# Kernel tuning notes

Hardware: AMD Instinct MI355X
Metric: run time of the kernel (lower is better)

Reference implementation:

```python
import math
import jax, jax.numpy as jnp
import numpy as np

EPS = 1e-5
NUM_HEADS = 8

def gelu(x):
    return jax.nn.gelu(x, approximate=False)  # keras 'gelu' is exact

def layernorm(x, g, b):
    m = jnp.mean(x, axis=-1, keepdims=True)
    v = jnp.var(x, axis=-1, keepdims=True)
    return (x - m) * jax.lax.rsqrt(v + EPS) * g + b

def setup_inputs() -> dict:
    key = jax.random.key(0)
    ks = jax.random.split(key, 12)
    B, S, N, D = 2, 1, 2048, 256
    E = 256  # dim_emb == dim_out
    s_in = 1.0 / np.sqrt(D).astype(np.float32)
    s_e = 1.0 / np.sqrt(E).astype(np.float32)
    s_h = 1.0 / np.sqrt(4 * E).astype(np.float32)
    return {
        "X": jax.random.normal(ks[0], (B, S, N, D), jnp.float32),
        "Wq": jax.random.normal(ks[1], (D, E), jnp.float32) * s_in,
        "Wk": jax.random.normal(ks[2], (D, E), jnp.float32) * s_in,
        "Wv": jax.random.normal(ks[3], (D, E), jnp.float32) * s_in,
        "Wm": jax.random.normal(ks[4], (E, E), jnp.float32) * s_e,
        "bm": jnp.zeros((E,), jnp.float32),
        "W1": jax.random.normal(ks[5], (E, 4 * E), jnp.float32) * s_e,
        "bf1": jnp.zeros((4 * E,), jnp.float32),
        "W2": jax.random.normal(ks[6], (4 * E, E), jnp.float32) * s_h,
        "bf2": jnp.zeros((E,), jnp.float32),
        "ln0_g": jnp.ones((D,), jnp.float32),
        "ln0_b": jnp.zeros((D,), jnp.float32),
        "ln1_g": jnp.ones((E,), jnp.float32),
        "ln1_b": jnp.zeros((E,), jnp.float32),
    }

def reference(X, Wq, Wk, Wv, Wm, bm, W1, bf1, W2, bf2, ln0_g, ln0_b, ln1_g, ln1_b):
    B, S, N, D = X.shape  # S == 1 (set-transformer singleton axis)
    E = Wq.shape[1]
    H = NUM_HEADS
    dh = E // H
    dim_KV = D  # softmax scale uses dim_KV, not head dim (faithful to source)

    # pre-layer-norm applies only to the Q branch; K/V use raw X
    Xn = layernorm(X, ln0_g, ln0_b)
    Q = Xn @ Wq                      # (B,1,N,E)
    K = X @ Wk
    V = X @ Wv
    X_res = Q                        # fc_res is None -> residual is Q

    def to_heads(T):                 # (B,1,N,E) -> (B,H,N,dh), split along last dim
        return T[:, 0].reshape(B, N, H, dh).transpose(0, 2, 1, 3)

    q, k, v = to_heads(Q), to_heads(K), to_heads(V)
    A = jnp.einsum('bhnd,bhmd->bhnm', q, k) * (1.0 / math.sqrt(dim_KV))  # (B,H,N,N)
    P = jax.nn.softmax(A, axis=-1)
    mh = jnp.einsum('bhnm,bhmd->bhnd', P, v)            # (B,H,N,dh)
    mh = mh.transpose(0, 2, 1, 3).reshape(B, 1, N, E)   # concat heads on last dim

    Hm = gelu(mh @ Wm + bm)          # fc_mix_heads has gelu activation
    H_after_res = Hm + X_res
    H_rff = layernorm(H_after_res, ln1_g, ln1_b)

    # rff: Dense(4E, gelu) then an extra explicit gelu, then Dense(E, gelu)
    h1 = gelu(gelu(H_rff @ W1 + bf1))
    h2 = gelu(h1 @ W2 + bf2)
    return H_after_res + h2
```

## Files before the change

kernel.cpp:

```cpp
#include <hip/hip_runtime.h>
#include <math.h>

#define NTOK 2048
#define EDIM 256
#define ROWS 4096
#define SLOT (ROWS * EDIM)

typedef __attribute__((ext_vector_type(8))) short bf16x8;
typedef __attribute__((ext_vector_type(4))) short bf16x4_t;
typedef __attribute__((ext_vector_type(4))) unsigned short u16x4;
typedef __attribute__((ext_vector_type(4))) float f32x4;
typedef __attribute__((ext_vector_type(4))) unsigned u32x4;
typedef __attribute__((ext_vector_type(2))) unsigned u32x2;

__device__ __forceinline__ float gelu_f(float x) {
    return 0.5f * x * (1.0f + erff(x * 0.70710678118654752f));
}
__device__ __forceinline__ unsigned short f2bf(float x) {
    unsigned u = __builtin_bit_cast(unsigned, x);
    u += 0x7FFFu + ((u >> 16) & 1u);
    return (unsigned short)(u >> 16);
}
__device__ __forceinline__ float bf2f(unsigned short h) {
    unsigned u = ((unsigned)h) << 16;
    return __builtin_bit_cast(float, u);
}
__device__ __forceinline__ unsigned pack2(float lo, float hi) {
    unsigned r;
    asm("v_cvt_pk_bf16_f32 %0, %1, %2" : "=v"(r) : "v"(lo), "v"(hi));
    return r;
}

__global__ __launch_bounds__(256) void prep(const float* __restrict__ Wq, const float* __restrict__ Wk,
                                            const float* __restrict__ Wv, const float* __restrict__ Wm,
                                            const float* __restrict__ W1, const float* __restrict__ W2,
                                            const float* __restrict__ X, const float* __restrict__ ln0g,
                                            const float* __restrict__ ln0b,
                                            unsigned short* WqT, unsigned short* WkvT,
                                            unsigned short* WmT, unsigned short* W1T,
                                            unsigned short* W2T,
                                            unsigned short* __restrict__ Xnb,
                                            unsigned short* __restrict__ Xb) {
    __shared__ float Ls[64][65];
    const int bid = blockIdx.x;
    if (bid < 192) {
        const float* src;
        unsigned short* dst;
        int K, N, t;
        if (bid < 16)       { src = Wq; dst = WqT;             K = 256;  N = 256;  t = bid; }
        else if (bid < 32)  { src = Wk; dst = WkvT;            K = 256;  N = 256;  t = bid - 16; }
        else if (bid < 48)  { src = Wv; dst = WkvT + 256*256;  K = 256;  N = 256;  t = bid - 32; }
        else if (bid < 64)  { src = Wm; dst = WmT;             K = 256;  N = 256;  t = bid - 48; }
        else if (bid < 128) { src = W1; dst = W1T;             K = 256;  N = 1024; t = bid - 64; }
        else                { src = W2; dst = W2T;             K = 1024; N = 256;  t = bid - 128; }
        const int tn = N >> 6;
        const int k0 = (t / tn) * 64, n0 = (t % tn) * 64;
        const int r = threadIdx.x >> 2, cq = threadIdx.x & 3;
#pragma unroll
        for (int u = 0; u < 4; ++u) {
            const float4 v = *(const float4*)&src[(size_t)(k0 + r) * N + n0 + cq * 16 + u * 4];
            Ls[r][cq * 16 + u * 4 + 0] = v.x;
            Ls[r][cq * 16 + u * 4 + 1] = v.y;
            Ls[r][cq * 16 + u * 4 + 2] = v.z;
            Ls[r][cq * 16 + u * 4 + 3] = v.w;
        }
        __syncthreads();
#pragma unroll
        for (int hh = 0; hh < 2; ++hh) {
            bf16x8 o;
#pragma unroll
            for (int j = 0; j < 8; ++j) o[j] = (short)f2bf(Ls[cq * 16 + hh * 8 + j][r]);
            *(bf16x8*)&dst[(size_t)(n0 + r) * K + k0 + cq * 16 + hh * 8] = o;
        }
    } else {
        const int wave = threadIdx.x >> 6, lane = threadIdx.x & 63;
        const int row = (bid - 192) * 4 + wave;
        const float4 v = *(const float4*)&X[(size_t)row * EDIM + lane * 4];
        float s = v.x + v.y + v.z + v.w;
        float s2 = v.x * v.x + v.y * v.y + v.z * v.z + v.w * v.w;
#pragma unroll
        for (int off = 1; off < 64; off <<= 1) {
            s += __shfl_xor(s, off);
            s2 += __shfl_xor(s2, off);
        }
        const float mean = s * (1.0f / 256.0f);
        const float var = s2 * (1.0f / 256.0f) - mean * mean;
        const float rstd = rsqrtf(var + 1e-5f);
        const float4 gg = *(const float4*)&ln0g[lane * 4];
        const float4 bb = *(const float4*)&ln0b[lane * 4];
        u16x4 o;
        o[0] = f2bf((v.x - mean) * rstd * gg.x + bb.x);
        o[1] = f2bf((v.y - mean) * rstd * gg.y + bb.y);
        o[2] = f2bf((v.z - mean) * rstd * gg.z + bb.z);
        o[3] = f2bf((v.w - mean) * rstd * gg.w + bb.w);
        *(u16x4*)&Xnb[(size_t)row * EDIM + lane * 4] = o;
        u16x4 rw;
        rw[0] = f2bf(v.x); rw[1] = f2bf(v.y); rw[2] = f2bf(v.z); rw[3] = f2bf(v.w);
        *(u16x4*)&Xb[(size_t)row * EDIM + lane * 4] = rw;
    }
}

template <bool RAW>
__global__ __launch_bounds__(256) void ln_bf16(const float* __restrict__ X, const float* __restrict__ g,
                                               const float* __restrict__ b, unsigned short* __restrict__ Y,
                                               unsigned short* __restrict__ Yraw) {
    const int wave = threadIdx.x >> 6, lane = threadIdx.x & 63;
    const int row = blockIdx.x * 4 + wave;
    const float4 v = *(const float4*)&X[(size_t)row * EDIM + lane * 4];
    float s = v.x + v.y + v.z + v.w;
    float s2 = v.x * v.x + v.y * v.y + v.z * v.z + v.w * v.w;
#pragma unroll
    for (int off = 1; off < 64; off <<= 1) {
        s += __shfl_xor(s, off);
        s2 += __shfl_xor(s2, off);
    }
    const float mean = s * (1.0f / 256.0f);
    const float var = s2 * (1.0f / 256.0f) - mean * mean;
    const float rstd = rsqrtf(var + 1e-5f);
    const float4 gg = *(const float4*)&g[lane * 4];
    const float4 bb = *(const float4*)&b[lane * 4];
    u16x4 o;
    o[0] = f2bf((v.x - mean) * rstd * gg.x + bb.x);
    o[1] = f2bf((v.y - mean) * rstd * gg.y + bb.y);
    o[2] = f2bf((v.z - mean) * rstd * gg.z + bb.z);
    o[3] = f2bf((v.w - mean) * rstd * gg.w + bb.w);
    *(u16x4*)&Y[(size_t)row * EDIM + lane * 4] = o;
    if (RAW) {
        u16x4 rw;
        rw[0] = f2bf(v.x); rw[1] = f2bf(v.y); rw[2] = f2bf(v.z); rw[3] = f2bf(v.w);
        *(u16x4*)&Yraw[(size_t)row * EDIM + lane * 4] = rw;
    }
}

template <int EPI, int BN>
__device__ __forceinline__ void gemm_body(const unsigned short* __restrict__ A,
                                          const unsigned short* __restrict__ Bt,
                                          const float* __restrict__ bias,
                                          const float* __restrict__ res,
                                          float* __restrict__ outF,
                                          unsigned short* __restrict__ outB,
                                          int N, int K, int bx, int by,
                                          unsigned short (*As)[72], unsigned short (*Bs)[72]) {
    constexpr int NI = BN / 32;
    const int tid = threadIdx.x;
    const int lane = tid & 63, wid = tid >> 6;
    const int c = lane & 15, g = lane >> 4;
    const int wm = wid & 1, wn = wid >> 1;
    const int row0 = by * 32, col0 = bx * BN;
    const int sarow = tid >> 3, saq = tid & 7;
    const int sbrow = tid >> 2, sbq = tid & 3;
    f32x4 acc[NI] = {};
    bf16x8 a_r = *(const bf16x8*)&A[(size_t)(row0 + sarow) * K + saq * 8];
    bf16x8 b_r0, b_r1;
    if (BN == 64) {
        const bf16x8* gb = (const bf16x8*)&Bt[(size_t)(col0 + sbrow) * K + sbq * 16];
        b_r0 = gb[0];
        b_r1 = gb[1];
    } else {
        b_r0 = *(const bf16x8*)&Bt[(size_t)(col0 + sarow) * K + saq * 8];
    }
    for (int k0 = 0; k0 < K; k0 += 64) {
        *(bf16x8*)&As[sarow][saq * 8] = a_r;
        if (BN == 64) {
            *(bf16x8*)&Bs[sbrow][sbq * 16] = b_r0;
            *(bf16x8*)&Bs[sbrow][sbq * 16 + 8] = b_r1;
        } else {
            *(bf16x8*)&Bs[sarow][saq * 8] = b_r0;
        }
        __syncthreads();
        if (k0 + 64 < K) {
            a_r = *(const bf16x8*)&A[(size_t)(row0 + sarow) * K + k0 + 64 + saq * 8];
            if (BN == 64) {
                const bf16x8* gb = (const bf16x8*)&Bt[(size_t)(col0 + sbrow) * K + k0 + 64 + sbq * 16];
                b_r0 = gb[0];
                b_r1 = gb[1];
            } else {
                b_r0 = *(const bf16x8*)&Bt[(size_t)(col0 + sarow) * K + k0 + 64 + saq * 8];
            }
        }
#pragma unroll
        for (int ks = 0; ks < 2; ++ks) {
            const bf16x8 af = *(const bf16x8*)&As[wm * 16 + c][ks * 32 + 8 * g];
#pragma unroll
            for (int ni = 0; ni < NI; ++ni) {
                const bf16x8 bv = *(const bf16x8*)&Bs[(wn * NI + ni) * 16 + c][ks * 32 + 8 * g];
                acc[ni] = __builtin_amdgcn_mfma_f32_16x16x32_bf16(af, bv, acc[ni], 0, 0, 0);
            }
        }
        __syncthreads();
    }
#pragma unroll
    for (int ni = 0; ni < NI; ++ni) {
        const int colx = col0 + (wn * NI + ni) * 16 + c;
        const float bi = (EPI != 0) ? bias[colx] : 0.0f;
#pragma unroll
        for (int r = 0; r < 4; ++r) {
            const int rowx = row0 + wm * 16 + 4 * g + r;
            const size_t idx = (size_t)rowx * N + colx;
            float v = acc[ni][r];
            if (EPI == 1) v = res[idx] + gelu_f(v + bi);
            else if (EPI == 2) v = gelu_f(gelu_f(v + bi));
            if (outF) outF[idx] = v;
            if (outB) outB[idx] = f2bf(v);
        }
    }
}

template <int EPI, int BN>
__global__ __launch_bounds__(256) void gemm_bf16(const unsigned short* __restrict__ A,
                                                 const unsigned short* __restrict__ Bt,
                                                 const float* __restrict__ bias,
                                                 const float* __restrict__ res,
                                                 float* __restrict__ outF,
                                                 unsigned short* __restrict__ outB,
                                                 int M, int N, int K) {
    __shared__ unsigned short As[32][72];
    __shared__ unsigned short Bs[BN][72];
    gemm_body<EPI, BN>(A, Bt, bias, res, outF, outB, N, K, blockIdx.x, blockIdx.y, As, Bs);
}

__global__ __launch_bounds__(256) void qkv_gemm(const unsigned short* __restrict__ Xnb,
                                                const unsigned short* __restrict__ Xb,
                                                const unsigned short* __restrict__ WqT,
                                                const unsigned short* __restrict__ WkvT,
                                                float* __restrict__ Qf,
                                                unsigned short* __restrict__ Qb,
                                                unsigned short* __restrict__ KVb) {
    __shared__ unsigned short As[32][72];
    __shared__ unsigned short Bs[64][72];
    if (blockIdx.y < 128)
        gemm_body<0, 32>(Xnb, WqT, nullptr, nullptr, Qf, Qb, 256, 256, blockIdx.x, blockIdx.y, As, Bs);
    else
        gemm_body<0, 64>(Xb, WkvT, nullptr, nullptr, nullptr, KVb, 512, 256, blockIdx.x, blockIdx.y - 128, As, Bs);
}

__global__ __launch_bounds__(256) void attn_mfma(const unsigned short* __restrict__ Qb,
                                                 const unsigned short* __restrict__ KVb,
                                                 unsigned short* __restrict__ Opart,
                                                 float* __restrict__ ML) {
    __shared__ char smem[18944];
    unsigned short (*Ks)[64][40] = (unsigned short (*)[64][40])smem;
    unsigned short (*Vt)[32][68] = (unsigned short (*)[32][68])(smem + 10240);
    float (*Otf)[16][36]         = (float (*)[16][36])smem;
    const int tid = threadIdx.x, lane = tid & 63, wid = tid >> 6;
    const int c = lane & 15, g = lane >> 4;
    const int bid = blockIdx.x;
    const int qt = bid & 31, h = (bid >> 5) & 7, b = (bid >> 8) & 1, s = bid >> 9;
    const int qrow = b * NTOK + qt * 64 + wid * 16;
    const int skey = tid >> 2, skq = tid & 3;
    const int vkp = tid & 31, vdq = tid >> 5;
    const int vk = (2 * vkp) & 31;
    const int vcol = ((2 * vkp) >> 5) * 32 + ((vk & 15) >> 2) * 8 + (vk >> 4) * 4 + (vk & 3);
    const size_t kvbase = (size_t)b * NTOK * 512 + h * 32;
    const int key0 = s * 512;

    bf16x8 qf;
    {
        const bf16x8 qraw = *(const bf16x8*)&Qb[(size_t)(qrow + c) * EDIM + h * 32 + 8 * g];
#pragma unroll
        for (int j = 0; j < 8; ++j)
            qf[j] = (short)f2bf(bf2f((unsigned short)qraw[j]) * 0.09016844f);
    }
    const f32x4 zero4 = {0.0f, 0.0f, 0.0f, 0.0f};
    f32x4 accO[2] = {zero4, zero4};
    float lsum = 0.0f;

    {
        const int c0 = key0;
        const bf16x8 kr = *(const bf16x8*)&KVb[kvbase + (size_t)(c0 + skey) * 512 + skq * 8];
        const u16x4 v0 = *(const u16x4*)&KVb[kvbase + (size_t)(c0 + 2 * vkp) * 512 + 256 + vdq * 4];
        const u16x4 v1 = *(const u16x4*)&KVb[kvbase + (size_t)(c0 + 2 * vkp + 1) * 512 + 256 + vdq * 4];
        *(bf16x8*)&Ks[0][skey][skq * 8] = kr;
#pragma unroll
        for (int i = 0; i < 4; ++i)
            *(unsigned*)&Vt[0][vdq * 4 + i][vcol] = ((unsigned)v1[i] << 16) | (unsigned)v0[i];
    }
    __syncthreads();

    for (int t = 0; t < 8; ++t) {
        const int cur = t & 1;
        bf16x8 kr2;
        u32x4 vr2;
        if (t < 7) {
            const int c0 = key0 + (t + 1) * 64;
            kr2 = *(const bf16x8*)&KVb[kvbase + (size_t)(c0 + skey) * 512 + skq * 8];
            const u16x4 v0 = *(const u16x4*)&KVb[kvbase + (size_t)(c0 + 2 * vkp) * 512 + 256 + vdq * 4];
            const u16x4 v1 = *(const u16x4*)&KVb[kvbase + (size_t)(c0 + 2 * vkp + 1) * 512 + 256 + vdq * 4];
#pragma unroll
            for (int i = 0; i < 4; ++i) vr2[i] = ((unsigned)v1[i] << 16) | (unsigned)v0[i];
        }

        f32x4 st[4];
        __builtin_amdgcn_s_setprio(1);
#pragma unroll
        for (int t4 = 0; t4 < 4; ++t4) {
            const bf16x8 kf = *(const bf16x8*)&Ks[cur][t4 * 16 + c][8 * g];
            st[t4] = __builtin_amdgcn_mfma_f32_16x16x32_bf16(kf, qf, zero4, 0, 0, 0);
        }
        __builtin_amdgcn_s_setprio(0);
#pragma unroll
        for (int t4 = 0; t4 < 4; ++t4)
#pragma unroll
            for (int r = 0; r < 4; ++r) {
                const float e = exp2f(st[t4][r]);
                st[t4][r] = e;
                lsum += e;
            }

        unsigned pk[8];
#pragma unroll
        for (int t4 = 0; t4 < 4; ++t4)
#pragma unroll
            for (int b2 = 0; b2 < 2; ++b2)
                pk[2 * t4 + b2] = pack2(st[t4][2 * b2], st[t4][2 * b2 + 1]);

        __builtin_amdgcn_s_setprio(1);
#pragma unroll
        for (int kc = 0; kc < 2; ++kc) {
            const u32x4 bw = {pk[4 * kc], pk[4 * kc + 1], pk[4 * kc + 2], pk[4 * kc + 3]};
            const bf16x8 bpv = __builtin_bit_cast(bf16x8, bw);
#pragma unroll
            for (int dt = 0; dt < 2; ++dt) {
                const bf16x4_t vlo = *(const bf16x4_t*)&Vt[cur][c + 16 * dt][8 * g + 32 * kc];
                const bf16x4_t vhi = *(const bf16x4_t*)&Vt[cur][c + 16 * dt][8 * g + 32 * kc + 4];
                const u32x2 L = __builtin_bit_cast(u32x2, vlo);
                const u32x2 H2 = __builtin_bit_cast(u32x2, vhi);
                const u32x4 q4 = {L[0], L[1], H2[0], H2[1]};
                const bf16x8 vf = __builtin_bit_cast(bf16x8, q4);
                accO[dt] = __builtin_amdgcn_mfma_f32_16x16x32_bf16(vf, bpv, accO[dt], 0, 0, 0);
            }
        }
        __builtin_amdgcn_s_setprio(0);

        if (t < 7) {
            *(bf16x8*)&Ks[cur ^ 1][skey][skq * 8] = kr2;
#pragma unroll
            for (int i = 0; i < 4; ++i)
                *(unsigned*)&Vt[cur ^ 1][vdq * 4 + i][vcol] = vr2[i];
            __syncthreads();
        }
    }

    lsum += __shfl_xor(lsum, 16);
    lsum += __shfl_xor(lsum, 32);
    __syncthreads();
    const float inv = 1.0f / lsum;
#pragma unroll
    for (int dt = 0; dt < 2; ++dt)
#pragma unroll
        for (int r = 0; r < 4; ++r)
            Otf[wid][c][dt * 16 + 4 * g + r] = accO[dt][r] * inv;
    if (g == 0) {
        ML[((size_t)s * 4096 + qrow + c) * 8 + h] = lsum;
    }
    const int oq = lane >> 2, odq = lane & 3;
    const float* srcp = &Otf[wid][oq][odq * 8];
    u32x4 packed;
    packed[0] = pack2(srcp[0], srcp[1]);
    packed[1] = pack2(srcp[2], srcp[3]);
    packed[2] = pack2(srcp[4], srcp[5]);
    packed[3] = pack2(srcp[6], srcp[7]);
    *(u32x4*)&Opart[(size_t)s * SLOT + (size_t)(qrow + oq) * EDIM + h * 32 + odq * 8] = packed;
}

__global__ __launch_bounds__(256) void attn_combine(const unsigned short* __restrict__ Opart,
                                                    const float* __restrict__ ML,
                                                    unsigned short* __restrict__ mhb) {
    const int flat4 = blockIdx.x * 256 + threadIdx.x;
    const int row = flat4 >> 6;
    const int col = (flat4 & 63) * 4;
    const int h = col >> 5;
    float lw[4];
    float lt = 0.0f;
#pragma unroll
    for (int s = 0; s < 4; ++s) {
        lw[s] = ML[((size_t)s * 4096 + row) * 8 + h];
        lt += lw[s];
    }
    const float inv = 1.0f / lt;
    float a[4] = {0.0f, 0.0f, 0.0f, 0.0f};
#pragma unroll
    for (int s = 0; s < 4; ++s) {
        const u16x4 p = *(const u16x4*)&Opart[(size_t)s * SLOT + (size_t)row * EDIM + col];
#pragma unroll
        for (int j = 0; j < 4; ++j) a[j] += lw[s] * bf2f((unsigned short)p[j]);
    }
    u16x4 r;
#pragma unroll
    for (int j = 0; j < 4; ++j) r[j] = f2bf(a[j] * inv);
    *(u16x4*)&mhb[(size_t)row * EDIM + col] = r;
}

extern "C" void kernel_launch(void* const* d_in, const int* in_sizes, int n_in,
                              void* d_out, int out_size, void* d_ws, size_t ws_size,
                              hipStream_t stream) {
    const float* X    = (const float*)d_in[0];
    const float* Wq   = (const float*)d_in[1];
    const float* Wk   = (const float*)d_in[2];
    const float* Wv   = (const float*)d_in[3];
    const float* Wm   = (const float*)d_in[4];
    const float* bm   = (const float*)d_in[5];
    const float* W1   = (const float*)d_in[6];
    const float* bf1  = (const float*)d_in[7];
    const float* W2   = (const float*)d_in[8];
    const float* bf2  = (const float*)d_in[9];
    const float* ln0g = (const float*)d_in[10];
    const float* ln0b = (const float*)d_in[11];
    const float* ln1g = (const float*)d_in[12];
    const float* ln1b = (const float*)d_in[13];
    float* out = (float*)d_out;
    char* w = (char*)d_ws;

    unsigned short* WqT  = (unsigned short*)(w + 0);
    unsigned short* WkvT = (unsigned short*)(w + 131072);
    unsigned short* WmT  = (unsigned short*)(w + 393216);
    unsigned short* W1T  = (unsigned short*)(w + 524288);
    unsigned short* W2T  = (unsigned short*)(w + 1048576);
    unsigned short* Xb   = (unsigned short*)(w + 1572864);
    float*          ML   = (float*)(w + 1572864);
    unsigned short* Xnb  = (unsigned short*)(w + 3670016);
    unsigned short* Qb   = (unsigned short*)(w + 5767168);
    float*          Qf   = (float*)(w + 7864320);
    unsigned short* KVb  = (unsigned short*)(w + 12058624);
    unsigned short* mhb  = (unsigned short*)(w + 16252928);
    float*          Hres = (float*)(w + 18350080);
    unsigned short* Hrff = (unsigned short*)(w + 22544384);
    unsigned short* h1b  = (unsigned short*)(w + 24641536);
    unsigned short* Opart= (unsigned short*)(w + 24641536);

    prep<<<1216, 256, 0, stream>>>(Wq, Wk, Wv, Wm, W1, W2, X, ln0g, ln0b,
                                   WqT, WkvT, WmT, W1T, W2T, Xnb, Xb);
    qkv_gemm<<<dim3(8, 256), 256, 0, stream>>>(Xnb, Xb, WqT, WkvT, Qf, Qb, KVb);
    attn_mfma<<<2048, 256, 0, stream>>>(Qb, KVb, Opart, ML);
    attn_combine<<<1024, 256, 0, stream>>>(Opart, ML, mhb);
    gemm_bf16<1, 32><<<dim3(8, 128), 256, 0, stream>>>(mhb, WmT, bm, Qf, Hres, nullptr, ROWS, 256, 256);
    ln_bf16<false><<<ROWS / 4, 256, 0, stream>>>(Hres, ln1g, ln1b, Hrff, nullptr);
    gemm_bf16<2, 64><<<dim3(16, 128), 256, 0, stream>>>(Hrff, W1T, bf1, nullptr, nullptr, h1b, ROWS, 1024, 256);
    gemm_bf16<1, 32><<<dim3(8, 128), 256, 0, stream>>>(h1b, W2T, bf2, Hres, out, nullptr, ROWS, 256, 1024);
}
```

Measured before the change: 86.89 us.

## Store residual intermediates in bf16 and double GEMM K-tile to 128

Drops the fp32 Q and H_after_res buffers. The residual path now reads bf16 Q and writes and reads a bf16 H_after_res, which roughly halves the memory traffic for those intermediates and removes one output stream from the QKV GEMM. The GEMM body also stages 128-wide K slices in shared memory instead of 64, which halves the number of barrier iterations at the cost of more LDS and registers per block. The final output's residual term now carries bf16 rounding error, which may reduce accuracy.

```diff
diff --git a/kernel.cpp b/kernel.cpp
--- a/kernel.cpp
+++ b/kernel.cpp
@@ -100,13 +100,15 @@
     }
 }
 
-template <bool RAW>
-__global__ __launch_bounds__(256) void ln_bf16(const float* __restrict__ X, const float* __restrict__ g,
-                                               const float* __restrict__ b, unsigned short* __restrict__ Y,
-                                               unsigned short* __restrict__ Yraw) {
+__global__ __launch_bounds__(256) void ln_bf16_in(const unsigned short* __restrict__ X,
+                                                  const float* __restrict__ g,
+                                                  const float* __restrict__ b,
+                                                  unsigned short* __restrict__ Y) {
     const int wave = threadIdx.x >> 6, lane = threadIdx.x & 63;
     const int row = blockIdx.x * 4 + wave;
-    const float4 v = *(const float4*)&X[(size_t)row * EDIM + lane * 4];
+    const u16x4 vh = *(const u16x4*)&X[(size_t)row * EDIM + lane * 4];
+    float4 v;
+    v.x = bf2f(vh[0]); v.y = bf2f(vh[1]); v.z = bf2f(vh[2]); v.w = bf2f(vh[3]);
     float s = v.x + v.y + v.z + v.w;
     float s2 = v.x * v.x + v.y * v.y + v.z * v.z + v.w * v.w;
 #pragma unroll
@@ -125,22 +127,17 @@
     o[2] = f2bf((v.z - mean) * rstd * gg.z + bb.z);
     o[3] = f2bf((v.w - mean) * rstd * gg.w + bb.w);
     *(u16x4*)&Y[(size_t)row * EDIM + lane * 4] = o;
-    if (RAW) {
-        u16x4 rw;
-        rw[0] = f2bf(v.x); rw[1] = f2bf(v.y); rw[2] = f2bf(v.z); rw[3] = f2bf(v.w);
-        *(u16x4*)&Yraw[(size_t)row * EDIM + lane * 4] = rw;
-    }
 }
 
 template <int EPI, int BN>
 __device__ __forceinline__ void gemm_body(const unsigned short* __restrict__ A,
                                           const unsigned short* __restrict__ Bt,
                                           const float* __restrict__ bias,
-                                          const float* __restrict__ res,
+                                          const unsigned short* __restrict__ resB,
                                           float* __restrict__ outF,
                                           unsigned short* __restrict__ outB,
                                           int N, int K, int bx, int by,
-                                          unsigned short (*As)[72], unsigned short (*Bs)[72]) {
+                                          unsigned short (*As)[136], unsigned short (*Bs)[136]) {
     constexpr int NI = BN / 32;
     const int tid = threadIdx.x;
     const int lane = tid & 63, wid = tid >> 6;
@@ -150,36 +147,44 @@
     const int sarow = tid >> 3, saq = tid & 7;
     const int sbrow = tid >> 2, sbq = tid & 3;
     f32x4 acc[NI] = {};
-    bf16x8 a_r = *(const bf16x8*)&A[(size_t)(row0 + sarow) * K + saq * 8];
-    bf16x8 b_r0, b_r1;
-    if (BN == 64) {
-        const bf16x8* gb = (const bf16x8*)&Bt[(size_t)(col0 + sbrow) * K + sbq * 16];
-        b_r0 = gb[0];
-        b_r1 = gb[1];
-    } else {
-        b_r0 = *(const bf16x8*)&Bt[(size_t)(col0 + sarow) * K + saq * 8];
-    }
-    for (int k0 = 0; k0 < K; k0 += 64) {
-        *(bf16x8*)&As[sarow][saq * 8] = a_r;
+    bf16x8 a_r0, a_r1, b_r0, b_r1, b_r2, b_r3;
+    {
+        const bf16x8* ga = (const bf16x8*)&A[(size_t)(row0 + sarow) * K + saq * 16];
+        a_r0 = ga[0]; a_r1 = ga[1];
         if (BN == 64) {
-            *(bf16x8*)&Bs[sbrow][sbq * 16] = b_r0;
-            *(bf16x8*)&Bs[sbrow][sbq * 16 + 8] = b_r1;
+            const bf16x8* gb = (const bf16x8*)&Bt[(size_t)(col0 + sbrow) * K + sbq * 32];
+            b_r0 = gb[0]; b_r1 = gb[1]; b_r2 = gb[2]; b_r3 = gb[3];
         } else {
-            *(bf16x8*)&Bs[sarow][saq * 8] = b_r0;
+            const bf16x8* gb = (const bf16x8*)&Bt[(size_t)(col0 + sarow) * K + saq * 16];
+            b_r0 = gb[0]; b_r1 = gb[1];
+        }
+    }
+    for (int k0 = 0; k0 < K; k0 += 128) {
+        *(bf16x8*)&As[sarow][saq * 16] = a_r0;
+        *(bf16x8*)&As[sarow][saq * 16 + 8] = a_r1;
+        if (BN == 64) {
+            *(bf16x8*)&Bs[sbrow][sbq * 32] = b_r0;
+            *(bf16x8*)&Bs[sbrow][sbq * 32 + 8] = b_r1;
+            *(bf16x8*)&Bs[sbrow][sbq * 32 + 16] = b_r2;
+            *(bf16x8*)&Bs[sbrow][sbq * 32 + 24] = b_r3;
+        } else {
+            *(bf16x8*)&Bs[sarow][saq * 16] = b_r0;
+            *(bf16x8*)&Bs[sarow][saq * 16 + 8] = b_r1;
         }
         __syncthreads();
-        if (k0 + 64 < K) {
-            a_r = *(const bf16x8*)&A[(size_t)(row0 + sarow) * K + k0 + 64 + saq * 8];
+        if (k0 + 128 < K) {
+            const bf16x8* ga = (const bf16x8*)&A[(size_t)(row0 + sarow) * K + k0 + 128 + saq * 16];
+            a_r0 = ga[0]; a_r1 = ga[1];
             if (BN == 64) {
-                const bf16x8* gb = (const bf16x8*)&Bt[(size_t)(col0 + sbrow) * K + k0 + 64 + sbq * 16];
-                b_r0 = gb[0];
-                b_r1 = gb[1];
+                const bf16x8* gb = (const bf16x8*)&Bt[(size_t)(col0 + sbrow) * K + k0 + 128 + sbq * 32];
+                b_r0 = gb[0]; b_r1 = gb[1]; b_r2 = gb[2]; b_r3 = gb[3];
             } else {
-                b_r0 = *(const bf16x8*)&Bt[(size_t)(col0 + sarow) * K + k0 + 64 + saq * 8];
+                const bf16x8* gb = (const bf16x8*)&Bt[(size_t)(col0 + sarow) * K + k0 + 128 + saq * 16];
+                b_r0 = gb[0]; b_r1 = gb[1];
             }
         }
 #pragma unroll
-        for (int ks = 0; ks < 2; ++ks) {
+        for (int ks = 0; ks < 4; ++ks) {
             const bf16x8 af = *(const bf16x8*)&As[wm * 16 + c][ks * 32 + 8 * g];
 #pragma unroll
             for (int ni = 0; ni < NI; ++ni) {
@@ -198,7 +203,7 @@
             const int rowx = row0 + wm * 16 + 4 * g + r;
             const size_t idx = (size_t)rowx * N + colx;
             float v = acc[ni][r];
-            if (EPI == 1) v = res[idx] + gelu_f(v + bi);
+            if (EPI == 1) v = bf2f(resB[idx]) + gelu_f(v + bi);
             else if (EPI == 2) v = gelu_f(gelu_f(v + bi));
             if (outF) outF[idx] = v;
             if (outB) outB[idx] = f2bf(v);
@@ -210,26 +215,25 @@
 __global__ __launch_bounds__(256) void gemm_bf16(const unsigned short* __restrict__ A,
                                                  const unsigned short* __restrict__ Bt,
                                                  const float* __restrict__ bias,
-                                                 const float* __restrict__ res,
+                                                 const unsigned short* __restrict__ resB,
                                                  float* __restrict__ outF,
                                                  unsigned short* __restrict__ outB,
                                                  int M, int N, int K) {
-    __shared__ unsigned short As[32][72];
-    __shared__ unsigned short Bs[BN][72];
-    gemm_body<EPI, BN>(A, Bt, bias, res, outF, outB, N, K, blockIdx.x, blockIdx.y, As, Bs);
+    __shared__ unsigned short As[32][136];
+    __shared__ unsigned short Bs[BN][136];
+    gemm_body<EPI, BN>(A, Bt, bias, resB, outF, outB, N, K, blockIdx.x, blockIdx.y, As, Bs);
 }
 
 __global__ __launch_bounds__(256) void qkv_gemm(const unsigned short* __restrict__ Xnb,
                                                 const unsigned short* __restrict__ Xb,
                                                 const unsigned short* __restrict__ WqT,
                                                 const unsigned short* __restrict__ WkvT,
-                                                float* __restrict__ Qf,
                                                 unsigned short* __restrict__ Qb,
                                                 unsigned short* __restrict__ KVb) {
-    __shared__ unsigned short As[32][72];
-    __shared__ unsigned short Bs[64][72];
+    __shared__ unsigned short As[32][136];
+    __shared__ unsigned short Bs[64][136];
     if (blockIdx.y < 128)
-        gemm_body<0, 32>(Xnb, WqT, nullptr, nullptr, Qf, Qb, 256, 256, blockIdx.x, blockIdx.y, As, Bs);
+        gemm_body<0, 32>(Xnb, WqT, nullptr, nullptr, nullptr, Qb, 256, 256, blockIdx.x, blockIdx.y, As, Bs);
     else
         gemm_body<0, 64>(Xb, WkvT, nullptr, nullptr, nullptr, KVb, 512, 256, blockIdx.x, blockIdx.y - 128, As, Bs);
 }
@@ -420,21 +424,20 @@
     float*          ML   = (float*)(w + 1572864);
     unsigned short* Xnb  = (unsigned short*)(w + 3670016);
     unsigned short* Qb   = (unsigned short*)(w + 5767168);
-    float*          Qf   = (float*)(w + 7864320);
     unsigned short* KVb  = (unsigned short*)(w + 12058624);
     unsigned short* mhb  = (unsigned short*)(w + 16252928);
-    float*          Hres = (float*)(w + 18350080);
+    unsigned short* HresB= (unsigned short*)(w + 18350080);
     unsigned short* Hrff = (unsigned short*)(w + 22544384);
     unsigned short* h1b  = (unsigned short*)(w + 24641536);
     unsigned short* Opart= (unsigned short*)(w + 24641536);
 
     prep<<<1216, 256, 0, stream>>>(Wq, Wk, Wv, Wm, W1, W2, X, ln0g, ln0b,
                                    WqT, WkvT, WmT, W1T, W2T, Xnb, Xb);
-    qkv_gemm<<<dim3(8, 256), 256, 0, stream>>>(Xnb, Xb, WqT, WkvT, Qf, Qb, KVb);
+    qkv_gemm<<<dim3(8, 256), 256, 0, stream>>>(Xnb, Xb, WqT, WkvT, Qb, KVb);
     attn_mfma<<<2048, 256, 0, stream>>>(Qb, KVb, Opart, ML);
     attn_combine<<<1024, 256, 0, stream>>>(Opart, ML, mhb);
-    gemm_bf16<1, 32><<<dim3(8, 128), 256, 0, stream>>>(mhb, WmT, bm, Qf, Hres, nullptr, ROWS, 256, 256);
-    ln_bf16<false><<<ROWS / 4, 256, 0, stream>>>(Hres, ln1g, ln1b, Hrff, nullptr);
+    gemm_bf16<1, 32><<<dim3(8, 128), 256, 0, stream>>>(mhb, WmT, bm, Qb, nullptr, HresB, ROWS, 256, 256);
+    ln_bf16_in<<<ROWS / 4, 256, 0, stream>>>(HresB, ln1g, ln1b, Hrff);
     gemm_bf16<2, 64><<<dim3(16, 128), 256, 0, stream>>>(Hrff, W1T, bf1, nullptr, nullptr, h1b, ROWS, 1024, 256);
-    gemm_bf16<1, 32><<<dim3(8, 128), 256, 0, stream>>>(h1b, W2T, bf2, Hres, out, nullptr, ROWS, 256, 1024);
-}
+    gemm_bf16<1, 32><<<dim3(8, 128), 256, 0, stream>>>(h1b, W2T, bf2, HresB, out, nullptr, ROWS, 256, 1024);
+}
```

After: 88.89 us. +2.3%, slower.
